# Kernel optimization log

Hardware: AMD Instinct MI355X
Metric: run time of the kernel (lower is better)

Reference implementation:

```python
import jax, jax.numpy as jnp
import numpy as np

N = 100000
E = 1600000
F_IN, H = 64, 128


def setup_inputs() -> dict:
    key = jax.random.key(0)
    ks = jax.random.split(key, 8)
    inp = {
        "x": jax.random.normal(ks[0], (N, F_IN), dtype=jnp.float32),
        "edge_index": jax.random.randint(ks[1], (2, E), 0, N, dtype=jnp.int64),
        "W1": jax.random.normal(ks[2], (F_IN, H), dtype=jnp.float32) / np.sqrt(F_IN),
        "b1": jnp.zeros((H,), jnp.float32),
        "W2": jax.random.normal(ks[3], (H, H), dtype=jnp.float32) / np.sqrt(H),
        "b2": jnp.zeros((H,), jnp.float32),
        "W3": jax.random.normal(ks[4], (H, H // 2), dtype=jnp.float32) / np.sqrt(H),
        "b3": jnp.zeros((H // 2,), jnp.float32),
        "Wc1": jax.random.normal(ks[5], (H // 2, H // 4), dtype=jnp.float32) / np.sqrt(H // 2),
        "bc1": jnp.zeros((H // 4,), jnp.float32),
        "Wc2": jax.random.normal(ks[6], (H // 4, 2), dtype=jnp.float32) / np.sqrt(H // 4),
        "bc2": jnp.zeros((2,), jnp.float32),
    }
    return inp


def _gcn_norm(edge_index, n):
    # PyG GCNConv default: add self-loops, symmetric D^-1/2 A_hat D^-1/2 norm
    loop = jnp.arange(n, dtype=edge_index.dtype)
    src = jnp.concatenate([edge_index[0], loop])
    dst = jnp.concatenate([edge_index[1], loop])
    deg = jax.ops.segment_sum(jnp.ones_like(dst, dtype=jnp.float32), dst, num_segments=n)
    dis = jax.lax.rsqrt(jnp.maximum(deg, 1.0))
    norm = dis[src] * dis[dst]  # [E+N]
    return src, dst, norm


def _gcn_conv(x, W, b, src, dst, norm, n):
    h = x @ W                      # [N, H_out]
    msg = h[src] * norm[:, None]   # gather + scale, [E+N, H_out]
    out = jax.ops.segment_sum(msg, dst, num_segments=n)  # scatter-add
    return out + b


def reference(x, edge_index, W1, b1, W2, b2, W3, b3, Wc1, bc1, Wc2, bc2):
    n = x.shape[0]
    src, dst, norm = _gcn_norm(edge_index, n)
    h1 = jax.nn.relu(_gcn_conv(x, W1, b1, src, dst, norm, n))
    h2 = jax.nn.relu(_gcn_conv(h1, W2, b2, src, dst, norm, n))
    h3 = jax.nn.relu(_gcn_conv(h2, W3, b3, src, dst, norm, n))
    pooled = jnp.mean(h3, axis=0, keepdims=True)  # [1, H//2]
    z = jax.nn.relu(pooled @ Wc1 + bc1)
    logits = z @ Wc2 + bc2
    return jax.nn.softmax(logits, axis=1)
```

## Files before the change

### kernel.cpp

```cpp
#include <hip/hip_runtime.h>

#define NN 100000
#define NE 1600000
#define NBUCKET 391
#define CHUNK 4096

typedef __attribute__((ext_vector_type(2))) float v2f;
typedef __attribute__((ext_vector_type(8))) short bf16x8;
typedef __attribute__((ext_vector_type(4))) float f32x4;


__device__ __forceinline__ unsigned int pk4fp8(float a, float b, float c, float d) {
    int t = __builtin_amdgcn_cvt_pk_fp8_f32(a, b, 0, false);
    t = __builtin_amdgcn_cvt_pk_fp8_f32(c, d, t, true);
    return (unsigned int)t;
}
__device__ __forceinline__ void acc4(unsigned int u, float* a) {
    v2f p0 = __builtin_amdgcn_cvt_pk_f32_fp8((int)u, false);
    v2f p1 = __builtin_amdgcn_cvt_pk_f32_fp8((int)u, true);
    a[0] += p0.x; a[1] += p0.y; a[2] += p1.x; a[3] += p1.y;
}
__device__ __forceinline__ void acc16(uint4 u, float* a) {
    acc4(u.x, a); acc4(u.y, a + 4); acc4(u.z, a + 8); acc4(u.w, a + 12);
}


__device__ __forceinline__ unsigned short f2b(float f) {
    unsigned int u; __builtin_memcpy(&u, &f, 4);
    unsigned int r = (u + 0x7fffu + ((u >> 16) & 1u)) >> 16;
    return (unsigned short)r;
}
__device__ __forceinline__ unsigned int pk2b(float a, float b) {
    return (unsigned int)f2b(a) | ((unsigned int)f2b(b) << 16);
}


__global__ void k_zero32(int* __restrict__ p, int n) {
    int i = blockIdx.x * 256 + threadIdx.x;
    if (i < n) p[i] = 0;
}

__global__ __launch_bounds__(256) void k_p1(const int* __restrict__ dst,
                                            int* __restrict__ bcnt, int E) {
    __shared__ int h[NBUCKET];
    for (int i = threadIdx.x; i < NBUCKET; i += 256) h[i] = 0;
    __syncthreads();
    int stride = gridDim.x * 256;
    for (int i = blockIdx.x * 256 + threadIdx.x; i < E; i += stride)
        atomicAdd(&h[dst[i] >> 8], 1);
    __syncthreads();
    for (int i = threadIdx.x; i < NBUCKET; i += 256)
        if (h[i]) atomicAdd(&bcnt[i], h[i]);
}

__global__ void k_scanb(const int* __restrict__ bcnt, int* __restrict__ bbase,
                        int* __restrict__ bfill) {
    __shared__ int s[512];
    int t = threadIdx.x;
    int v = (t < NBUCKET) ? bcnt[t] : 0;
    s[t] = v; __syncthreads();
    for (int off = 1; off < 512; off <<= 1) {
        int x = (t >= off) ? s[t - off] : 0;
        __syncthreads();
        s[t] += x;
        __syncthreads();
    }
    if (t < NBUCKET) { int ex = s[t] - v; bbase[t] = ex; bfill[t] = ex; }
    if (t == NBUCKET) bbase[t] = s[511];
}

__global__ __launch_bounds__(256) void k_p2(const int* __restrict__ src,
                                            const int* __restrict__ dst,
                                            int* __restrict__ bfill,
                                            unsigned int* __restrict__ entries, int E) {
    __shared__ int h[NBUCKET];
    __shared__ int cur[NBUCKET];
    int c0 = blockIdx.x * CHUNK;
    int c1 = min(E, c0 + CHUNK);
    for (int i = threadIdx.x; i < NBUCKET; i += 256) h[i] = 0;
    __syncthreads();
    for (int i = c0 + threadIdx.x; i < c1; i += 256) atomicAdd(&h[dst[i] >> 8], 1);
    __syncthreads();
    for (int i = threadIdx.x; i < NBUCKET; i += 256)
        cur[i] = h[i] ? atomicAdd(&bfill[i], h[i]) : 0;
    __syncthreads();
    for (int i = c0 + threadIdx.x; i < c1; i += 256) {
        int d = dst[i];
        int bkt = d >> 8;
        int pos = atomicAdd(&cur[bkt], 1);
        entries[pos] = (unsigned int)src[i] | ((unsigned int)(d & 255) << 17);
    }
}

__global__ __launch_bounds__(256) void k_p4x(const unsigned int* __restrict__ entries,
                                             const int* __restrict__ bbase,
                                             int* __restrict__ row_ptr,
                                             float* __restrict__ dis,
                                             int* __restrict__ col,
                                             const float4* __restrict__ x4,
                                             uint2* __restrict__ xb2, int N) {
    __shared__ int cnt[256];
    __shared__ int cur[256];
    __shared__ int sc[256];
    __shared__ float sdis[256];
    int b = blockIdx.x;
    int e0 = bbase[b], e1 = bbase[b + 1];
    int t = threadIdx.x;
    cnt[t] = 0; __syncthreads();
    for (int i = e0 + t; i < e1; i += 256)
        atomicAdd(&cnt[(entries[i] >> 17) & 255], 1);
    __syncthreads();
    int v = cnt[t];
    sc[t] = v; __syncthreads();
    for (int off = 1; off < 256; off <<= 1) {
        int x = (t >= off) ? sc[t - off] : 0;
        __syncthreads();
        sc[t] += x;
        __syncthreads();
    }
    int ex = sc[t] - v;
    int n = (b << 8) + t;
    float dv = rsqrtf((float)(v + 1));
    if (n <= N) row_ptr[n] = e0 + ex;
    if (n < N) dis[n] = dv;
    sdis[t] = dv;
    cur[t] = e0 + ex;
    __syncthreads();
    for (int i = e0 + t; i < e1; i += 256) {
        unsigned int en = entries[i];
        int pos = atomicAdd(&cur[(en >> 17) & 255], 1);
        col[pos] = (int)(en & 0x1FFFF);
    }
    for (int idx = t; idx < 256 * 8; idx += 256) {
        int node = idx >> 3, k = idx & 7;
        int gn = (b << 8) + node;
        if (gn < N) {
            float s = sdis[node];
            float4 A = x4[gn * 16 + 2 * k];
            float4 B = x4[gn * 16 + 2 * k + 1];
            uint2 u;
            u.x = pk4fp8(A.x * s, A.y * s, A.z * s, A.w * s);
            u.y = pk4fp8(B.x * s, B.y * s, B.z * s, B.w * s);
            xb2[gn * 8 + k] = u;
        }
    }
}

__global__ __launch_bounds__(256) void k_wcvt(
    const float* __restrict__ W1, const float* __restrict__ W2,
    const float* __restrict__ W3, uint4* __restrict__ Wp) {
    int t = blockIdx.x * 256 + threadIdx.x;
    const float* W; int Dout, e, base;
    if (t < 1024)       { W = W1; Dout = 128; e = t;        base = 0; }
    else if (t < 3072)  { W = W2; Dout = 128; e = t - 1024; base = 1024; }
    else                { W = W3; Dout = 64;  e = t - 3072; base = 3072; }
    int k4q = e / Dout, ch = e % Dout;
    int k0 = (k4q >> 2) * 32 + (k4q & 3) * 8;
    float v[8];
    #pragma unroll
    for (int j = 0; j < 8; j++) v[j] = W[(k0 + j) * Dout + ch];
    uint4 u;
    u.x = pk2b(v[0], v[1]); u.y = pk2b(v[2], v[3]);
    u.z = pk2b(v[4], v[5]); u.w = pk2b(v[6], v[7]);
    Wp[base + e] = u;
}


__global__ __launch_bounds__(256) void k_agg64s(
    const uint4* __restrict__ g4, const int* __restrict__ row_ptr,
    const int* __restrict__ col, const float* __restrict__ dis,
    uint4* __restrict__ outb, int N) {
    int tid = threadIdx.x;
    int lane = tid & 63, wave = tid >> 6;
    int slot = lane >> 2, seg = lane & 3;
    int n = blockIdx.x * 64 + wave * 16 + slot;
    if (n >= N) return;
    int b = row_ptr[n], e = row_ptr[n + 1];
    float a[16];
    #pragma unroll
    for (int q = 0; q < 16; q++) a[q] = 0.f;
    acc16(g4[n * 4 + seg], a);
    int i = b;
    for (; i + 4 <= e; i += 4) {
        int c0 = col[i], c1 = col[i + 1], c2 = col[i + 2], c3 = col[i + 3];
        uint4 u0 = g4[c0 * 4 + seg], u1 = g4[c1 * 4 + seg];
        uint4 u2 = g4[c2 * 4 + seg], u3 = g4[c3 * 4 + seg];
        acc16(u0, a); acc16(u1, a); acc16(u2, a); acc16(u3, a);
    }
    for (; i < e; i++) acc16(g4[col[i] * 4 + seg], a);
    float s = dis[n];
    uint4 u0, u1;
    u0.x = pk2b(s*a[0],  s*a[1]);  u0.y = pk2b(s*a[2],  s*a[3]);
    u0.z = pk2b(s*a[4],  s*a[5]);  u0.w = pk2b(s*a[6],  s*a[7]);
    u1.x = pk2b(s*a[8],  s*a[9]);  u1.y = pk2b(s*a[10], s*a[11]);
    u1.z = pk2b(s*a[12], s*a[13]); u1.w = pk2b(s*a[14], s*a[15]);
    outb[n * 8 + seg * 2]     = u0;
    outb[n * 8 + seg * 2 + 1] = u1;
}

__global__ __launch_bounds__(256) void k_agg128s(
    const uint4* __restrict__ g4, const int* __restrict__ row_ptr,
    const int* __restrict__ col, const float* __restrict__ dis,
    uint4* __restrict__ outb, int N) {
    int tid = threadIdx.x;
    int lane = tid & 63, wave = tid >> 6;
    int slot = lane >> 3, seg = lane & 7;
    int n = blockIdx.x * 32 + wave * 8 + slot;
    if (n >= N) return;
    int b = row_ptr[n], e = row_ptr[n + 1];
    float a[16];
    #pragma unroll
    for (int q = 0; q < 16; q++) a[q] = 0.f;
    acc16(g4[n * 8 + seg], a);
    int i = b;
    for (; i + 4 <= e; i += 4) {
        int c0 = col[i], c1 = col[i + 1], c2 = col[i + 2], c3 = col[i + 3];
        uint4 u0 = g4[c0 * 8 + seg], u1 = g4[c1 * 8 + seg];
        uint4 u2 = g4[c2 * 8 + seg], u3 = g4[c3 * 8 + seg];
        acc16(u0, a); acc16(u1, a); acc16(u2, a); acc16(u3, a);
    }
    for (; i < e; i++) acc16(g4[col[i] * 8 + seg], a);
    float s = dis[n];
    uint4 u0, u1;
    u0.x = pk2b(s*a[0],  s*a[1]);  u0.y = pk2b(s*a[2],  s*a[3]);
    u0.z = pk2b(s*a[4],  s*a[5]);  u0.w = pk2b(s*a[6],  s*a[7]);
    u1.x = pk2b(s*a[8],  s*a[9]);  u1.y = pk2b(s*a[10], s*a[11]);
    u1.z = pk2b(s*a[12], s*a[13]); u1.w = pk2b(s*a[14], s*a[15]);
    outb[n * 16 + seg * 2]     = u0;
    outb[n * 16 + seg * 2 + 1] = u1;
}

__global__ __launch_bounds__(256) void k_aggpools(
    const uint4* __restrict__ g4, const int* __restrict__ row_ptr,
    const int* __restrict__ col, const float* __restrict__ dis,
    const float* __restrict__ b3, float* __restrict__ partial, int N) {
    int tid = threadIdx.x;
    int lane = tid & 63, wave = tid >> 6;
    int slot = lane >> 2, seg = lane & 3;
    int n = blockIdx.x * 64 + wave * 16 + slot;
    float ap[16];
    #pragma unroll
    for (int j = 0; j < 16; j++) ap[j] = 0.f;
    if (n < N) {
        int b = row_ptr[n], e = row_ptr[n + 1];
        float a[16];
        #pragma unroll
        for (int q = 0; q < 16; q++) a[q] = 0.f;
        acc16(g4[n * 4 + seg], a);
        int i = b;
        for (; i + 4 <= e; i += 4) {
            int c0 = col[i], c1 = col[i + 1], c2 = col[i + 2], c3 = col[i + 3];
            uint4 u0 = g4[c0 * 4 + seg], u1 = g4[c1 * 4 + seg];
            uint4 u2 = g4[c2 * 4 + seg], u3 = g4[c3 * 4 + seg];
            acc16(u0, a); acc16(u1, a); acc16(u2, a); acc16(u3, a);
        }
        for (; i < e; i++) acc16(g4[col[i] * 4 + seg], a);
        float s = dis[n];
        #pragma unroll
        for (int j = 0; j < 16; j++)
            ap[j] = fmaxf(s * a[j] + b3[seg * 16 + j], 0.f);
    }
    #pragma unroll
    for (int j = 0; j < 16; j++) {
        ap[j] += __shfl_xor(ap[j], 4);
        ap[j] += __shfl_xor(ap[j], 8);
        ap[j] += __shfl_xor(ap[j], 16);
        ap[j] += __shfl_xor(ap[j], 32);
    }
    __shared__ float red[4][64];
    if (slot == 0) {
        #pragma unroll
        for (int j = 0; j < 16; j++) red[wave][seg * 16 + j] = ap[j];
    }
    __syncthreads();
    if (tid < 64)
        partial[blockIdx.x * 64 + tid] =
            red[0][tid] + red[1][tid] + red[2][tid] + red[3][tid];
}

template <int Din, int Dout, int OUTM>
__global__ __launch_bounds__(256) void k_mmx(
    const uint4* __restrict__ Xb,
    const uint4* __restrict__ Wp,
    const float* __restrict__ bias, const float* __restrict__ dis,
    void* __restrict__ outv, int N) {
    constexpr int KT = Din / 32;
    constexpr int CT = Dout / 16;
    const int tid = threadIdx.x, wave = tid >> 6, lane = tid & 63;
    const int quad = lane >> 4, l16 = lane & 15;
    const int node = blockIdx.x * 64 + wave * 16 + l16;
    const bool valid = node < N;
    const int nc = valid ? node : (N - 1);
    bf16x8 bfrag[KT];
    const uint4* xrow = Xb + (size_t)nc * (Din / 8);
    #pragma unroll
    for (int kt = 0; kt < KT; kt++) {
        uint4 u = xrow[kt * 4 + quad];
        bfrag[kt] = *(bf16x8*)&u;
    }
    const float s = (OUTM != 3 && valid) ? dis[node] : 0.f;
    #pragma unroll
    for (int ct = 0; ct < CT; ct++) {
        f32x4 c = {0.f, 0.f, 0.f, 0.f};
        #pragma unroll
        for (int kt = 0; kt < KT; kt++) {
            uint4 wu = Wp[(kt * 4 + quad) * Dout + ct * 16 + l16];
            bf16x8 afrag = *(bf16x8*)&wu;
            c = __builtin_amdgcn_mfma_f32_16x16x32_bf16(afrag, bfrag[kt], c, 0, 0, 0);
        }
        if (valid) {
            const int chb = ct * 16 + quad * 4;
            float r0 = c[0], r1 = c[1], r2 = c[2], r3 = c[3];
            if (OUTM != 3) {
                r0 = fmaxf(r0 + bias[chb + 0], 0.f) * s;
                r1 = fmaxf(r1 + bias[chb + 1], 0.f) * s;
                r2 = fmaxf(r2 + bias[chb + 2], 0.f) * s;
                r3 = fmaxf(r3 + bias[chb + 3], 0.f) * s;
            }
            if (OUTM == 1) {
                uint2 u; u.x = pk2b(r0, r1); u.y = pk2b(r2, r3);
                ((uint2*)outv)[(size_t)node * (Dout / 4) + ct * 4 + quad] = u;
            } else {
                ((unsigned int*)outv)[(size_t)node * (Dout / 4) + ct * 4 + quad] =
                    pk4fp8(r0, r1, r2, r3);
            }
        }
    }
}

__global__ __launch_bounds__(256) void k_red(
    const float* __restrict__ partial, float* __restrict__ partial2, int NB) {
    int blk = blockIdx.x;
    int t = threadIdx.x;
    int lane = t & 63, grp = t >> 6;
    int start = blk * 16;
    int end = min(NB, start + 16);
    float s = 0.f;
    for (int b = start + grp; b < end; b += 4) s += partial[b * 64 + lane];
    __shared__ float red[256];
    red[t] = s; __syncthreads();
    if (t < 64)
        partial2[blk * 64 + t] = red[t] + red[t + 64] + red[t + 128] + red[t + 192];
}

__global__ __launch_bounds__(256) void k_head(
    const float* __restrict__ partial, const float* __restrict__ Wc1,
    const float* __restrict__ bc1, const float* __restrict__ Wc2,
    const float* __restrict__ bc2, float* __restrict__ out, int NB, float invN) {
    __shared__ float red[256];
    __shared__ float pooled[64];
    __shared__ float z[32];
    __shared__ float lg[2];
    int t = threadIdx.x;
    int lane = t & 63, grp = t >> 6;
    float s = 0.f;
    for (int b = grp; b < NB; b += 4) s += partial[b * 64 + lane];
    red[t] = s; __syncthreads();
    if (t < 64) pooled[t] = (red[t] + red[t + 64] + red[t + 128] + red[t + 192]) * invN;
    __syncthreads();
    if (t < 32) {
        float a = bc1[t];
        for (int l = 0; l < 64; l++) a += pooled[l] * Wc1[l * 32 + t];
        z[t] = fmaxf(a, 0.f);
    }
    __syncthreads();
    if (t < 2) {
        float a = bc2[t];
        for (int j = 0; j < 32; j++) a += z[j] * Wc2[j * 2 + t];
        lg[t] = a;
    }
    __syncthreads();
    if (t == 0) {
        float m = fmaxf(lg[0], lg[1]);
        float e0 = __expf(lg[0] - m), e1 = __expf(lg[1] - m);
        float inv = 1.f / (e0 + e1);
        out[0] = e0 * inv;
        out[1] = e1 * inv;
    }
}


extern "C" void kernel_launch(void* const* d_in, const int* in_sizes, int n_in,
                              void* d_out, int out_size, void* d_ws, size_t ws_size,
                              hipStream_t stream) {
    (void)in_sizes; (void)n_in; (void)out_size; (void)ws_size;
    const int N = NN, E = NE;

    const float* x   = (const float*)d_in[0];
    const int*   ei  = (const int*)d_in[1];
    const int*   srcp = ei;
    const int*   dstp = ei + E;
    const float* W1 = (const float*)d_in[2];
    const float* b1 = (const float*)d_in[3];
    const float* W2 = (const float*)d_in[4];
    const float* b2 = (const float*)d_in[5];
    const float* W3 = (const float*)d_in[6];
    const float* b3 = (const float*)d_in[7];
    const float* Wc1 = (const float*)d_in[8];
    const float* bc1 = (const float*)d_in[9];
    const float* Wc2 = (const float*)d_in[10];
    const float* bc2 = (const float*)d_in[11];
    float* out = (float*)d_out;

    char* base = (char*)d_ws;
    size_t off = 0;
    auto carve = [&](size_t bytes) -> char* {
        char* p = base + off;
        off = (off + bytes + 255) & ~(size_t)255;
        return p;
    };
    int*   bcnt    = (int*)carve((size_t)NBUCKET * 4);
    int*   bbase   = (int*)carve((size_t)(NBUCKET + 1) * 4);
    int*   bfill   = (int*)carve((size_t)NBUCKET * 4);
    int*   row_ptr = (int*)carve((size_t)(N + 1) * 4);
    int*   col     = (int*)carve((size_t)E * 4);
    float* dis     = (float*)carve((size_t)N * 4);
    float* partial = (float*)carve((size_t)1600 * 64 * 4);
    float* partial2= (float*)carve((size_t)128 * 64 * 4);
    uint4* Wp      = (uint4*)carve((size_t)4096 * 16);
    unsigned int* entries = (unsigned int*)carve((size_t)E * 4);
    unsigned int* xb      = (unsigned int*)carve((size_t)N * 64);
    unsigned int* h1u     = (unsigned int*)carve((size_t)N * 128);
    uint4*        h2b     = (uint4*)carve((size_t)N * 128 * 2);
    unsigned int* g3u     = (unsigned int*)carve((size_t)N * 64);
    uint4*        bufB    = (uint4*)carve((size_t)N * 128 * 2);

    k_zero32<<<(NBUCKET + 255) / 256, 256, 0, stream>>>(bcnt, NBUCKET);
    k_p1<<<512, 256, 0, stream>>>(dstp, bcnt, E);
    k_scanb<<<1, 512, 0, stream>>>(bcnt, bbase, bfill);
    k_p2<<<(E + CHUNK - 1) / CHUNK, 256, 0, stream>>>(srcp, dstp, bfill, entries, E);
    k_wcvt<<<16, 256, 0, stream>>>(W1, W2, W3, Wp);
    k_p4x<<<NBUCKET, 256, 0, stream>>>(entries, bbase, row_ptr, dis, col,
                                       (const float4*)x, (uint2*)xb, N);

    const int NB64 = (N + 63) / 64;
    const int NB32 = (N + 31) / 32;

    k_agg64s<<<NB64, 256, 0, stream>>>((const uint4*)xb, row_ptr, col, dis, bufB, N);
    k_mmx<64, 128, 2><<<NB64, 256, 0, stream>>>(bufB, Wp, b1, dis, h1u, N);

    k_agg128s<<<NB32, 256, 0, stream>>>((const uint4*)h1u, row_ptr, col, dis, bufB, N);
    k_mmx<128, 128, 1><<<NB64, 256, 0, stream>>>(bufB, Wp + 1024, b2, dis, h2b, N);

    k_mmx<128, 64, 3><<<NB64, 256, 0, stream>>>(h2b, Wp + 3072, nullptr, nullptr, g3u, N);
    k_aggpools<<<NB64, 256, 0, stream>>>((const uint4*)g3u, row_ptr, col, dis, b3, partial, N);

    const int NRED = (NB64 + 15) / 16;
    k_red<<<NRED, 256, 0, stream>>>(partial, partial2, NB64);
    k_head<<<1, 256, 0, stream>>>(partial2, Wc1, bc1, Wc2, bc2, out, NRED, 1.0f / (float)N);
}
```

Before: 303.9 us.

## Fuse layer-1 aggregation with its GEMM, chain layer-2/3 GEMMs, merge init kernels

Layer-1 aggregation now stages its bf16 result in LDS and runs the W1 MFMA GEMM in the same kernel, so the intermediate buffer never goes to global memory. The layer-2 and layer-3 dense transforms are fused, with the ReLU'd h2 kept in LDS instead of being written out and read back. The bucket-count zeroing and weight-conversion kernels are merged into a single init launch. This removes several global round trips and kernel launches, at the cost of more LDS per block and a block-wide barrier.

```diff
diff --git a/kernel.cpp b/kernel.cpp
--- a/kernel.cpp
+++ b/kernel.cpp
@@ -34,11 +34,31 @@
     return (unsigned int)f2b(a) | ((unsigned int)f2b(b) << 16);
 }
 
-
-__global__ void k_zero32(int* __restrict__ p, int n) {
-    int i = blockIdx.x * 256 + threadIdx.x;
-    if (i < n) p[i] = 0;
-}
+__global__ __launch_bounds__(256) void k_init(
+    const float* __restrict__ W1, const float* __restrict__ W2,
+    const float* __restrict__ W3, uint4* __restrict__ Wp,
+    int* __restrict__ bcnt) {
+    int t = blockIdx.x * 256 + threadIdx.x;
+    if (t < 4096) {
+        const float* W; int Dout, e, base;
+        if (t < 1024)       { W = W1; Dout = 128; e = t;        base = 0; }
+        else if (t < 3072)  { W = W2; Dout = 128; e = t - 1024; base = 1024; }
+        else                { W = W3; Dout = 64;  e = t - 3072; base = 3072; }
+        int k4q = e / Dout, ch = e % Dout;
+        int k0 = (k4q >> 2) * 32 + (k4q & 3) * 8;
+        float v[8];
+        #pragma unroll
+        for (int j = 0; j < 8; j++) v[j] = W[(k0 + j) * Dout + ch];
+        uint4 u;
+        u.x = pk2b(v[0], v[1]); u.y = pk2b(v[2], v[3]);
+        u.z = pk2b(v[4], v[5]); u.w = pk2b(v[6], v[7]);
+        Wp[base + e] = u;
+    } else {
+        int i = t - 4096;
+        if (i < NBUCKET) bcnt[i] = 0;
+    }
+}
+
 
 __global__ __launch_bounds__(256) void k_p1(const int* __restrict__ dst,
                                             int* __restrict__ bcnt, int E) {
@@ -146,56 +166,66 @@
     }
 }
 
-__global__ __launch_bounds__(256) void k_wcvt(
-    const float* __restrict__ W1, const float* __restrict__ W2,
-    const float* __restrict__ W3, uint4* __restrict__ Wp) {
-    int t = blockIdx.x * 256 + threadIdx.x;
-    const float* W; int Dout, e, base;
-    if (t < 1024)       { W = W1; Dout = 128; e = t;        base = 0; }
-    else if (t < 3072)  { W = W2; Dout = 128; e = t - 1024; base = 1024; }
-    else                { W = W3; Dout = 64;  e = t - 3072; base = 3072; }
-    int k4q = e / Dout, ch = e % Dout;
-    int k0 = (k4q >> 2) * 32 + (k4q & 3) * 8;
-    float v[8];
-    #pragma unroll
-    for (int j = 0; j < 8; j++) v[j] = W[(k0 + j) * Dout + ch];
-    uint4 u;
-    u.x = pk2b(v[0], v[1]); u.y = pk2b(v[2], v[3]);
-    u.z = pk2b(v[4], v[5]); u.w = pk2b(v[6], v[7]);
-    Wp[base + e] = u;
-}
-
-
-__global__ __launch_bounds__(256) void k_agg64s(
-    const uint4* __restrict__ g4, const int* __restrict__ row_ptr,
+__global__ __launch_bounds__(256) void k_l1f(
+    const uint4* __restrict__ xb4, const int* __restrict__ row_ptr,
     const int* __restrict__ col, const float* __restrict__ dis,
-    uint4* __restrict__ outb, int N) {
-    int tid = threadIdx.x;
-    int lane = tid & 63, wave = tid >> 6;
-    int slot = lane >> 2, seg = lane & 3;
-    int n = blockIdx.x * 64 + wave * 16 + slot;
-    if (n >= N) return;
-    int b = row_ptr[n], e = row_ptr[n + 1];
+    const uint4* __restrict__ Wp, const float* __restrict__ b1,
+    unsigned int* __restrict__ h1u, int N) {
+    __shared__ unsigned short lds[4][16][72];
+    const int tid = threadIdx.x, lane = tid & 63, wave = tid >> 6;
+    const int slot = lane >> 2, seg = lane & 3;
+    const int n = blockIdx.x * 64 + wave * 16 + slot;
     float a[16];
     #pragma unroll
     for (int q = 0; q < 16; q++) a[q] = 0.f;
-    acc16(g4[n * 4 + seg], a);
-    int i = b;
-    for (; i + 4 <= e; i += 4) {
-        int c0 = col[i], c1 = col[i + 1], c2 = col[i + 2], c3 = col[i + 3];
-        uint4 u0 = g4[c0 * 4 + seg], u1 = g4[c1 * 4 + seg];
-        uint4 u2 = g4[c2 * 4 + seg], u3 = g4[c3 * 4 + seg];
-        acc16(u0, a); acc16(u1, a); acc16(u2, a); acc16(u3, a);
-    }
-    for (; i < e; i++) acc16(g4[col[i] * 4 + seg], a);
-    float s = dis[n];
+    if (n < N) {
+        int b = row_ptr[n], e = row_ptr[n + 1];
+        acc16(xb4[n * 4 + seg], a);
+        int i = b;
+        for (; i + 4 <= e; i += 4) {
+            int c0 = col[i], c1 = col[i + 1], c2 = col[i + 2], c3 = col[i + 3];
+            uint4 u0 = xb4[c0 * 4 + seg], u1 = xb4[c1 * 4 + seg];
+            uint4 u2 = xb4[c2 * 4 + seg], u3 = xb4[c3 * 4 + seg];
+            acc16(u0, a); acc16(u1, a); acc16(u2, a); acc16(u3, a);
+        }
+        for (; i < e; i++) acc16(xb4[col[i] * 4 + seg], a);
+        float s = dis[n];
+        #pragma unroll
+        for (int q = 0; q < 16; q++) a[q] *= s;
+    }
     uint4 u0, u1;
-    u0.x = pk2b(s*a[0],  s*a[1]);  u0.y = pk2b(s*a[2],  s*a[3]);
-    u0.z = pk2b(s*a[4],  s*a[5]);  u0.w = pk2b(s*a[6],  s*a[7]);
-    u1.x = pk2b(s*a[8],  s*a[9]);  u1.y = pk2b(s*a[10], s*a[11]);
-    u1.z = pk2b(s*a[12], s*a[13]); u1.w = pk2b(s*a[14], s*a[15]);
-    outb[n * 8 + seg * 2]     = u0;
-    outb[n * 8 + seg * 2 + 1] = u1;
+    u0.x = pk2b(a[0],  a[1]);  u0.y = pk2b(a[2],  a[3]);
+    u0.z = pk2b(a[4],  a[5]);  u0.w = pk2b(a[6],  a[7]);
+    u1.x = pk2b(a[8],  a[9]);  u1.y = pk2b(a[10], a[11]);
+    u1.z = pk2b(a[12], a[13]); u1.w = pk2b(a[14], a[15]);
+    *(uint4*)&lds[wave][slot][seg * 16]     = u0;
+    *(uint4*)&lds[wave][slot][seg * 16 + 8] = u1;
+    __syncthreads();
+    const int quad = lane >> 4, l16 = lane & 15;
+    const int node = blockIdx.x * 64 + wave * 16 + l16;
+    const bool valid = node < N;
+    bf16x8 bfrag[2];
+    #pragma unroll
+    for (int kt = 0; kt < 2; kt++)
+        bfrag[kt] = *(bf16x8*)&lds[wave][l16][kt * 32 + quad * 8];
+    const float s2 = valid ? dis[node] : 0.f;
+    #pragma unroll
+    for (int ct = 0; ct < 8; ct++) {
+        f32x4 c = {0.f, 0.f, 0.f, 0.f};
+        #pragma unroll
+        for (int kt = 0; kt < 2; kt++) {
+            uint4 wu = Wp[(kt * 4 + quad) * 128 + ct * 16 + l16];
+            c = __builtin_amdgcn_mfma_f32_16x16x32_bf16(*(bf16x8*)&wu, bfrag[kt], c, 0, 0, 0);
+        }
+        if (valid) {
+            const int chb = ct * 16 + quad * 4;
+            float r0 = fmaxf(c[0] + b1[chb + 0], 0.f) * s2;
+            float r1 = fmaxf(c[1] + b1[chb + 1], 0.f) * s2;
+            float r2 = fmaxf(c[2] + b1[chb + 2], 0.f) * s2;
+            float r3 = fmaxf(c[3] + b1[chb + 3], 0.f) * s2;
+            h1u[(size_t)node * 32 + ct * 4 + quad] = pk4fp8(r0, r1, r2, r3);
+        }
+    }
 }
 
 __global__ __launch_bounds__(256) void k_agg128s(
@@ -230,6 +260,59 @@
     outb[n * 16 + seg * 2 + 1] = u1;
 }
 
+__global__ __launch_bounds__(256) void k_mm23(
+    const uint4* __restrict__ Xb,
+    const uint4* __restrict__ Wp2, const uint4* __restrict__ Wp3,
+    const float* __restrict__ b2, const float* __restrict__ dis,
+    unsigned int* __restrict__ g3u, int N) {
+    __shared__ unsigned short lds[4][16][136];
+    const int tid = threadIdx.x, lane = tid & 63, wave = tid >> 6;
+    const int quad = lane >> 4, l16 = lane & 15;
+    const int node = blockIdx.x * 64 + wave * 16 + l16;
+    const bool valid = node < N;
+    const int nc = valid ? node : (N - 1);
+    bf16x8 bfrag[4];
+    const uint4* xrow = Xb + (size_t)nc * 16;
+    #pragma unroll
+    for (int kt = 0; kt < 4; kt++) {
+        uint4 u = xrow[kt * 4 + quad];
+        bfrag[kt] = *(bf16x8*)&u;
+    }
+    const float s = valid ? dis[node] : 0.f;
+    #pragma unroll
+    for (int ct = 0; ct < 8; ct++) {
+        f32x4 c = {0.f, 0.f, 0.f, 0.f};
+        #pragma unroll
+        for (int kt = 0; kt < 4; kt++) {
+            uint4 wu = Wp2[(kt * 4 + quad) * 128 + ct * 16 + l16];
+            c = __builtin_amdgcn_mfma_f32_16x16x32_bf16(*(bf16x8*)&wu, bfrag[kt], c, 0, 0, 0);
+        }
+        const int chb = ct * 16 + quad * 4;
+        float r0 = fmaxf(c[0] + b2[chb + 0], 0.f) * s;
+        float r1 = fmaxf(c[1] + b2[chb + 1], 0.f) * s;
+        float r2 = fmaxf(c[2] + b2[chb + 2], 0.f) * s;
+        float r3 = fmaxf(c[3] + b2[chb + 3], 0.f) * s;
+        uint2 u; u.x = pk2b(r0, r1); u.y = pk2b(r2, r3);
+        *(uint2*)&lds[wave][l16][chb] = u;
+    }
+    __syncthreads();
+    bf16x8 b2frag[4];
+    #pragma unroll
+    for (int kt = 0; kt < 4; kt++)
+        b2frag[kt] = *(bf16x8*)&lds[wave][l16][kt * 32 + quad * 8];
+    #pragma unroll
+    for (int ct = 0; ct < 4; ct++) {
+        f32x4 c = {0.f, 0.f, 0.f, 0.f};
+        #pragma unroll
+        for (int kt = 0; kt < 4; kt++) {
+            uint4 wu = Wp3[(kt * 4 + quad) * 64 + ct * 16 + l16];
+            c = __builtin_amdgcn_mfma_f32_16x16x32_bf16(*(bf16x8*)&wu, b2frag[kt], c, 0, 0, 0);
+        }
+        if (valid)
+            g3u[(size_t)node * 16 + ct * 4 + quad] = pk4fp8(c[0], c[1], c[2], c[3]);
+    }
+}
+
 __global__ __launch_bounds__(256) void k_aggpools(
     const uint4* __restrict__ g4, const int* __restrict__ row_ptr,
     const int* __restrict__ col, const float* __restrict__ dis,
@@ -276,56 +359,6 @@
     if (tid < 64)
         partial[blockIdx.x * 64 + tid] =
             red[0][tid] + red[1][tid] + red[2][tid] + red[3][tid];
-}
-
-template <int Din, int Dout, int OUTM>
-__global__ __launch_bounds__(256) void k_mmx(
-    const uint4* __restrict__ Xb,
-    const uint4* __restrict__ Wp,
-    const float* __restrict__ bias, const float* __restrict__ dis,
-    void* __restrict__ outv, int N) {
-    constexpr int KT = Din / 32;
-    constexpr int CT = Dout / 16;
-    const int tid = threadIdx.x, wave = tid >> 6, lane = tid & 63;
-    const int quad = lane >> 4, l16 = lane & 15;
-    const int node = blockIdx.x * 64 + wave * 16 + l16;
-    const bool valid = node < N;
-    const int nc = valid ? node : (N - 1);
-    bf16x8 bfrag[KT];
-    const uint4* xrow = Xb + (size_t)nc * (Din / 8);
-    #pragma unroll
-    for (int kt = 0; kt < KT; kt++) {
-        uint4 u = xrow[kt * 4 + quad];
-        bfrag[kt] = *(bf16x8*)&u;
-    }
-    const float s = (OUTM != 3 && valid) ? dis[node] : 0.f;
-    #pragma unroll
-    for (int ct = 0; ct < CT; ct++) {
-        f32x4 c = {0.f, 0.f, 0.f, 0.f};
-        #pragma unroll
-        for (int kt = 0; kt < KT; kt++) {
-            uint4 wu = Wp[(kt * 4 + quad) * Dout + ct * 16 + l16];
-            bf16x8 afrag = *(bf16x8*)&wu;
-            c = __builtin_amdgcn_mfma_f32_16x16x32_bf16(afrag, bfrag[kt], c, 0, 0, 0);
-        }
-        if (valid) {
-            const int chb = ct * 16 + quad * 4;
-            float r0 = c[0], r1 = c[1], r2 = c[2], r3 = c[3];
-            if (OUTM != 3) {
-                r0 = fmaxf(r0 + bias[chb + 0], 0.f) * s;
-                r1 = fmaxf(r1 + bias[chb + 1], 0.f) * s;
-                r2 = fmaxf(r2 + bias[chb + 2], 0.f) * s;
-                r3 = fmaxf(r3 + bias[chb + 3], 0.f) * s;
-            }
-            if (OUTM == 1) {
-                uint2 u; u.x = pk2b(r0, r1); u.y = pk2b(r2, r3);
-                ((uint2*)outv)[(size_t)node * (Dout / 4) + ct * 4 + quad] = u;
-            } else {
-                ((unsigned int*)outv)[(size_t)node * (Dout / 4) + ct * 4 + quad] =
-                    pk4fp8(r0, r1, r2, r3);
-            }
-        }
-    }
 }
 
 __global__ __launch_bounds__(256) void k_red(
@@ -421,28 +454,24 @@
     unsigned int* entries = (unsigned int*)carve((size_t)E * 4);
     unsigned int* xb      = (unsigned int*)carve((size_t)N * 64);
     unsigned int* h1u     = (unsigned int*)carve((size_t)N * 128);
-    uint4*        h2b     = (uint4*)carve((size_t)N * 128 * 2);
     unsigned int* g3u     = (unsigned int*)carve((size_t)N * 64);
     uint4*        bufB    = (uint4*)carve((size_t)N * 128 * 2);
 
-    k_zero32<<<(NBUCKET + 255) / 256, 256, 0, stream>>>(bcnt, NBUCKET);
+    k_init<<<18, 256, 0, stream>>>(W1, W2, W3, Wp, bcnt);
     k_p1<<<512, 256, 0, stream>>>(dstp, bcnt, E);
     k_scanb<<<1, 512, 0, stream>>>(bcnt, bbase, bfill);
     k_p2<<<(E + CHUNK - 1) / CHUNK, 256, 0, stream>>>(srcp, dstp, bfill, entries, E);
-    k_wcvt<<<16, 256, 0, stream>>>(W1, W2, W3, Wp);
     k_p4x<<<NBUCKET, 256, 0, stream>>>(entries, bbase, row_ptr, dis, col,
                                        (const float4*)x, (uint2*)xb, N);
 
     const int NB64 = (N + 63) / 64;
     const int NB32 = (N + 31) / 32;
 
-    k_agg64s<<<NB64, 256, 0, stream>>>((const uint4*)xb, row_ptr, col, dis, bufB, N);
-    k_mmx<64, 128, 2><<<NB64, 256, 0, stream>>>(bufB, Wp, b1, dis, h1u, N);
+    k_l1f<<<NB64, 256, 0, stream>>>((const uint4*)xb, row_ptr, col, dis, Wp, b1, h1u, N);
 
     k_agg128s<<<NB32, 256, 0, stream>>>((const uint4*)h1u, row_ptr, col, dis, bufB, N);
-    k_mmx<128, 128, 1><<<NB64, 256, 0, stream>>>(bufB, Wp + 1024, b2, dis, h2b, N);
-
-    k_mmx<128, 64, 3><<<NB64, 256, 0, stream>>>(h2b, Wp + 3072, nullptr, nullptr, g3u, N);
+    k_mm23<<<NB64, 256, 0, stream>>>(bufB, Wp + 1024, Wp + 3072, b2, dis, g3u, N);
+
     k_aggpools<<<NB64, 256, 0, stream>>>((const uint4*)g3u, row_ptr, col, dis, b3, partial, N);
 
     const int NRED = (NB64 + 15) / 16;
```

After: 281.9 us. 1.08x faster.
